# Kernel tuning notes

Hardware: AMD Instinct MI355X
Metric: run time of the kernel (lower is better)

## Reference

```python
import jax, jax.numpy as jnp
import numpy as np

N = 8192        # num nodes, > sparse_attention_threshold=5000 -> sparse attention path
IN = 128        # in_channels
OUT = 128       # out_channels
HEADS = 2       # attention_heads
DEG = 32        # avg degree used to build theta sparsity


def _xavier(key, shape):
    a = np.sqrt(6.0 / (shape[0] + shape[1])).astype(np.float32)
    return jax.random.uniform(key, shape, jnp.float32, -a, a)


def setup_inputs() -> dict:
    rng = np.random.default_rng(0)
    rows = np.repeat(np.arange(N), DEG)
    cols = rng.integers(0, N, size=N * DEG)
    theta_np = np.zeros((N, N), dtype=np.float32)
    theta_np[rows, cols] = 1.0
    # matches torch: rows, cols = np.where(theta > 1e-5)
    r, c = np.nonzero(theta_np > 1e-5)
    edge_index = jnp.asarray(np.stack([r, c]).astype(np.int32))  # [2, E]
    key = jax.random.key(0)
    ks = jax.random.split(key, 4)
    x = jax.random.normal(ks[0], (N, IN), jnp.float32)
    weight = _xavier(ks[1], (IN, OUT * HEADS))
    bias = jnp.zeros((OUT * HEADS,), jnp.float32)
    att_weight1 = _xavier(ks[2], (2 * OUT, OUT // 2))
    att_weight2 = _xavier(ks[3], (OUT // 2, 1))
    return {"x": x, "theta": jnp.asarray(theta_np), "weight": weight,
            "bias": bias, "att_weight1": att_weight1,
            "att_weight2": att_weight2, "edge_index": edge_index}


def _forward(x, weight, bias, att_weight1, att_weight2, edge_index):
    # x @ W + b, reshape to [N, heads, out]
    h = (x @ weight + bias).reshape(N, HEADS, OUT)
    src, dst = edge_index[0], edge_index[1]
    # cat([h_src, h_dst]) @ W1 == h_src @ W1[:OUT] + h_dst @ W1[OUT:]
    # project at node level first (cheaper), then gather per edge
    p_src = jnp.einsum('nhd,df->nhf', h, att_weight1[:OUT])
    p_dst = jnp.einsum('nhd,df->nhf', h, att_weight1[OUT:])
    s = jax.nn.leaky_relu(p_src[src] + p_dst[dst])               # [E, H, OUT//2]
    scores = jnp.einsum('ehf,fo->eho', s, att_weight2)[..., 0]    # [E, H]
    # torch does F.softmax(att_scores, dim=0): GLOBAL softmax over all edges per head
    att = jax.nn.softmax(scores, axis=0)                          # [E, H]
    # sparse COO mm: out[src] += att * h[dst]
    msgs = att[:, :, None] * h[dst]                               # [E, H, OUT]
    agg = jnp.zeros((N, HEADS, OUT), h.dtype).at[src].add(msgs)
    return agg.mean(axis=1)                                       # mean over heads -> [N, OUT]


def reference(x, theta, weight, bias, att_weight1, att_weight2, edge_index):
    # theta only determines the edge list (computed on CPU/numpy in the torch
    # code); edge_index is precomputed consistently in setup_inputs.
    del theta
    return _forward(x, weight, bias, att_weight1, att_weight2, edge_index)
```

## Files before the change

kernel.cpp:

```cpp
#include <hip/hip_runtime.h>
#include <hip/hip_bf16.h>

#define NN 8192
#define INC 128
#define HC 256
#define NPB 16
#define NGRP (NN / NPB)
#define APB 4
#define AGRID (NN / APB)
#define SCALE_BLOCKS 512
#define MAXDEG 32

__global__ __launch_bounds__(256) void k_h_p(
    const float* __restrict__ x, const float* __restrict__ W,
    const float* __restrict__ bias, const float* __restrict__ att1,
    const int* __restrict__ ei, float* __restrict__ h,
    float* __restrict__ ps, float* __restrict__ pd,
    int* __restrict__ offs, int E) {
  int t = threadIdx.x;
  int n0 = blockIdx.x * NPB;
  for (int e = blockIdx.x * 256 + t; e < E; e += NGRP * 256) {
    if (e == 0) offs[0] = 0;
    else { int s1 = ei[e]; if (s1 != ei[e - 1]) offs[s1] = e; }
    if (e == E - 1) offs[NN] = E;
  }
  __shared__ float xs[NPB * INC];
  __shared__ float hs[NPB * HC];
  {
    const float4* xin = (const float4*)(x + (size_t)n0 * INC);
    ((float4*)xs)[t] = xin[t];
    ((float4*)xs)[t + 256] = xin[t + 256];
  }
  __syncthreads();
  int cg = t & 63, ng = t >> 6;
  {
    float4 b4 = *(const float4*)&bias[cg * 4];
    float4 a0 = b4, a1 = b4, a2 = b4, a3 = b4;
    const float* xr0 = xs + (ng * 4 + 0) * INC;
    const float* xr1 = xs + (ng * 4 + 1) * INC;
    const float* xr2 = xs + (ng * 4 + 2) * INC;
    const float* xr3 = xs + (ng * 4 + 3) * INC;
    #pragma unroll 2
    for (int d = 0; d < INC; d += 4) {
      float4 xv0 = *(const float4*)&xr0[d];
      float4 xv1 = *(const float4*)&xr1[d];
      float4 xv2 = *(const float4*)&xr2[d];
      float4 xv3 = *(const float4*)&xr3[d];
      const float* f0 = (const float*)&xv0;
      const float* f1 = (const float*)&xv1;
      const float* f2 = (const float*)&xv2;
      const float* f3 = (const float*)&xv3;
      #pragma unroll
      for (int k = 0; k < 4; ++k) {
        float4 w4 = *(const float4*)&W[(size_t)(d + k) * HC + cg * 4];
        float x0 = f0[k], x1 = f1[k], x2 = f2[k], x3 = f3[k];
        a0.x += x0 * w4.x; a0.y += x0 * w4.y; a0.z += x0 * w4.z; a0.w += x0 * w4.w;
        a1.x += x1 * w4.x; a1.y += x1 * w4.y; a1.z += x1 * w4.z; a1.w += x1 * w4.w;
        a2.x += x2 * w4.x; a2.y += x2 * w4.y; a2.z += x2 * w4.z; a2.w += x2 * w4.w;
        a3.x += x3 * w4.x; a3.y += x3 * w4.y; a3.z += x3 * w4.z; a3.w += x3 * w4.w;
      }
    }
    float4* hb = (float4*)&hs[(ng * 4) * HC + cg * 4];
    *(float4*)&h[(size_t)(n0 + ng * 4 + 0) * HC + cg * 4] = a0;
    *(float4*)&h[(size_t)(n0 + ng * 4 + 1) * HC + cg * 4] = a1;
    *(float4*)&h[(size_t)(n0 + ng * 4 + 2) * HC + cg * 4] = a2;
    *(float4*)&h[(size_t)(n0 + ng * 4 + 3) * HC + cg * 4] = a3;
    hb[0] = a0; hb[HC / 4] = a1; hb[2 * HC / 4] = a2; hb[3 * HC / 4] = a3;
  }
  __syncthreads();
  {
    int fg = cg & 15, sel = cg >> 4;
    int head = sel & 1, isdst = sel >> 1;
    const float* a1p = att1 + isdst * 128 * 64 + fg * 4;
    float4 p0 = {0,0,0,0}, p1 = {0,0,0,0}, p2 = {0,0,0,0}, p3 = {0,0,0,0};
    const float* hr0 = hs + (ng * 4 + 0) * HC + head * 128;
    const float* hr1 = hs + (ng * 4 + 1) * HC + head * 128;
    const float* hr2 = hs + (ng * 4 + 2) * HC + head * 128;
    const float* hr3 = hs + (ng * 4 + 3) * HC + head * 128;
    #pragma unroll 2
    for (int d = 0; d < 128; d += 4) {
      float4 hv0 = *(const float4*)&hr0[d];
      float4 hv1 = *(const float4*)&hr1[d];
      float4 hv2 = *(const float4*)&hr2[d];
      float4 hv3 = *(const float4*)&hr3[d];
      const float* g0 = (const float*)&hv0;
      const float* g1 = (const float*)&hv1;
      const float* g2 = (const float*)&hv2;
      const float* g3 = (const float*)&hv3;
      #pragma unroll
      for (int k = 0; k < 4; ++k) {
        float4 a4 = *(const float4*)&a1p[(size_t)(d + k) * 64];
        float h0 = g0[k], h1 = g1[k], h2 = g2[k], h3 = g3[k];
        p0.x += h0 * a4.x; p0.y += h0 * a4.y; p0.z += h0 * a4.z; p0.w += h0 * a4.w;
        p1.x += h1 * a4.x; p1.y += h1 * a4.y; p1.z += h1 * a4.z; p1.w += h1 * a4.w;
        p2.x += h2 * a4.x; p2.y += h2 * a4.y; p2.z += h2 * a4.z; p2.w += h2 * a4.w;
        p3.x += h3 * a4.x; p3.y += h3 * a4.y; p3.z += h3 * a4.z; p3.w += h3 * a4.w;
      }
    }
    float* dp = isdst ? pd : ps;
    *(float4*)&dp[(size_t)(n0 + ng * 4 + 0) * 128 + head * 64 + fg * 4] = p0;
    *(float4*)&dp[(size_t)(n0 + ng * 4 + 1) * 128 + head * 64 + fg * 4] = p1;
    *(float4*)&dp[(size_t)(n0 + ng * 4 + 2) * 128 + head * 64 + fg * 4] = p2;
    *(float4*)&dp[(size_t)(n0 + ng * 4 + 3) * 128 + head * 64 + fg * 4] = p3;
  }
}

__global__ __launch_bounds__(256) void k_agg(
    const float* __restrict__ h, const float* __restrict__ ps,
    const float* __restrict__ pd, const int* __restrict__ ei,
    const float* __restrict__ att2, const int* __restrict__ offs,
    float* __restrict__ raw, float* __restrict__ part, int E) {
  int t = threadIdx.x, wid = t >> 6, lane = t & 63;
  int n = blockIdx.x * APB + wid;
  __shared__ float w2l[64];
  __shared__ int   dstl[APB][MAXDEG];
  if (t < 64) w2l[t] = att2[t];
  int lo = offs[n], hi = offs[n + 1];
  int m = hi - lo;
  if (lane < m) dstl[wid][lane] = ei[E + lo + lane];
  __syncthreads();
  int head = lane >> 5, j = lane & 31;
  float2 psv = *(const float2*)&ps[(size_t)n * 128 + head * 64 + j * 2];
  float wa = w2l[j * 2], wb = w2l[j * 2 + 1];
  float rsum = 0.f;
  float4 a0 = {0, 0, 0, 0}, a1 = {0, 0, 0, 0};
  int i = 0;
  #pragma unroll 2
  for (; i + 2 <= m; i += 2) {
    int d0 = dstl[wid][i], d1 = dstl[wid][i + 1];
    float2 q0 = *(const float2*)&pd[(size_t)d0 * 128 + head * 64 + j * 2];
    float2 q1 = *(const float2*)&pd[(size_t)d1 * 128 + head * 64 + j * 2];
    float4 h0 = *(const float4*)&h[(size_t)d0 * HC + lane * 4];
    float4 h1 = *(const float4*)&h[(size_t)d1 * HC + lane * 4];
    float u0 = psv.x + q0.x; u0 = u0 > 0.f ? u0 : 0.01f * u0;
    float u1 = psv.y + q0.y; u1 = u1 > 0.f ? u1 : 0.01f * u1;
    float s0 = u0 * wa + u1 * wb;
    float v0 = psv.x + q1.x; v0 = v0 > 0.f ? v0 : 0.01f * v0;
    float v1 = psv.y + q1.y; v1 = v1 > 0.f ? v1 : 0.01f * v1;
    float s1 = v0 * wa + v1 * wb;
    s0 += __shfl_xor(s0, 1);  s0 += __shfl_xor(s0, 2);  s0 += __shfl_xor(s0, 4);
    s0 += __shfl_xor(s0, 8);  s0 += __shfl_xor(s0, 16);
    s1 += __shfl_xor(s1, 1);  s1 += __shfl_xor(s1, 2);  s1 += __shfl_xor(s1, 4);
    s1 += __shfl_xor(s1, 8);  s1 += __shfl_xor(s1, 16);
    float e0 = __expf(s0), e1 = __expf(s1);
    rsum += e0; rsum += e1;
    a0.x += e0 * h0.x; a0.y += e0 * h0.y; a0.z += e0 * h0.z; a0.w += e0 * h0.w;
    a1.x += e1 * h1.x; a1.y += e1 * h1.y; a1.z += e1 * h1.z; a1.w += e1 * h1.w;
  }
  if (i < m) {
    int d0 = dstl[wid][i];
    float2 q0 = *(const float2*)&pd[(size_t)d0 * 128 + head * 64 + j * 2];
    float4 h0 = *(const float4*)&h[(size_t)d0 * HC + lane * 4];
    float u0 = psv.x + q0.x; u0 = u0 > 0.f ? u0 : 0.01f * u0;
    float u1 = psv.y + q0.y; u1 = u1 > 0.f ? u1 : 0.01f * u1;
    float s0 = u0 * wa + u1 * wb;
    s0 += __shfl_xor(s0, 1);  s0 += __shfl_xor(s0, 2);  s0 += __shfl_xor(s0, 4);
    s0 += __shfl_xor(s0, 8);  s0 += __shfl_xor(s0, 16);
    float e0 = __expf(s0);
    rsum += e0;
    a0.x += e0 * h0.x; a0.y += e0 * h0.y; a0.z += e0 * h0.z; a0.w += e0 * h0.w;
  }
  if (j == 0) part[n * 2 + head] = rsum;
  float4 res;
  res.x = a0.x + a1.x; res.y = a0.y + a1.y;
  res.z = a0.z + a1.z; res.w = a0.w + a1.w;
  *(float4*)&raw[(size_t)n * HC + lane * 4] = res;
}

__global__ __launch_bounds__(256) void k_scale(
    const float* __restrict__ raw, const float* __restrict__ part,
    float* __restrict__ out) {
  int t = threadIdx.x;
  float s0 = 0.f, s1 = 0.f;
  #pragma unroll 4
  for (int k = 0; k < 32; ++k) {
    float2 p = ((const float2*)part)[t + 256 * k];
    s0 += p.x; s1 += p.y;
  }
  #pragma unroll
  for (int off = 1; off <= 32; off <<= 1) {
    s0 += __shfl_xor(s0, off);
    s1 += __shfl_xor(s1, off);
  }
  __shared__ float ws0[4], ws1[4];
  if ((t & 63) == 0) { ws0[t >> 6] = s0; ws1[t >> 6] = s1; }
  __syncthreads();
  float inv0 = 1.f / (ws0[0] + ws0[1] + ws0[2] + ws0[3]);
  float inv1 = 1.f / (ws1[0] + ws1[1] + ws1[2] + ws1[3]);
  const float4* r4 = (const float4*)raw;
  float4* o4 = (float4*)out;
  int idx = blockIdx.x * 256 + t;
  #pragma unroll
  for (int rep = 0; rep < 2; ++rep, idx += SCALE_BLOCKS * 256) {
    int nn = idx >> 5, c4 = idx & 31;
    float4 a = r4[nn * 64 + c4];
    float4 b = r4[nn * 64 + 32 + c4];
    float4 o;
    o.x = 0.5f * (a.x * inv0 + b.x * inv1);
    o.y = 0.5f * (a.y * inv0 + b.y * inv1);
    o.z = 0.5f * (a.z * inv0 + b.z * inv1);
    o.w = 0.5f * (a.w * inv0 + b.w * inv1);
    o4[idx] = o;
  }
}

extern "C" void kernel_launch(void* const* d_in, const int* in_sizes, int n_in,
                              void* d_out, int out_size, void* d_ws, size_t ws_size,
                              hipStream_t stream) {
  const float* x    = (const float*)d_in[0];
  const float* W    = (const float*)d_in[2];
  const float* bias = (const float*)d_in[3];
  const float* att1 = (const float*)d_in[4];
  const float* att2 = (const float*)d_in[5];
  const int* ei = (const int*)d_in[6];
  int E = in_sizes[6] / 2;
  float* out = (float*)d_out;

  float* ws = (float*)d_ws;
  float* h    = ws;
  float* ps   = h  + (size_t)NN * HC;
  float* pd   = ps + (size_t)NN * 128;
  float* raw  = pd + (size_t)NN * 128;
  float* part = raw + (size_t)NN * HC;
  int*   offs = (int*)(part + (size_t)NN * 2);

  k_h_p<<<NGRP, 256, 0, stream>>>(x, W, bias, att1, ei, h, ps, pd, offs, E);
  k_agg<<<AGRID, 256, 0, stream>>>(h, ps, pd, ei, att2, offs, raw, part, E);
  k_scale<<<SCALE_BLOCKS, 256, 0, stream>>>(raw, part, out);
}
```

Measured before the change: 364.6 us.

## Split aggregation across head and channel-half blocks with XCD-aware mapping

The aggregation kernel now launches four times as many blocks, each handling one (head, channel-half) pair for a group of nodes, so each wave lane holds one scalar channel instead of a float4. Block indices are decoded so that all blocks on a given XCD (bid & 7) share the same head/channel combination, which is meant to keep that XCD's L2 working set to one column slice of h and pd. The cost is that the score computation, including the pd gather, is repeated for each channel half. Loads also shrink from float4 to scalar per lane.

```diff
diff --git a/kernel.cpp b/kernel.cpp
--- a/kernel.cpp
+++ b/kernel.cpp
@@ -7,7 +7,7 @@
 #define NPB 16
 #define NGRP (NN / NPB)
 #define APB 4
-#define AGRID (NN / APB)
+#define AGRID ((NN / APB) * 4)
 #define SCALE_BLOCKS 512
 #define MAXDEG 32
 
@@ -111,7 +111,12 @@
     const float* __restrict__ att2, const int* __restrict__ offs,
     float* __restrict__ raw, float* __restrict__ part, int E) {
   int t = threadIdx.x, wid = t >> 6, lane = t & 63;
-  int n = blockIdx.x * APB + wid;
+  int bid = blockIdx.x;
+  int xcd = bid & 7;
+  int combo = xcd >> 1;
+  int head = combo >> 1, ch = combo & 1;
+  int gidx = ((bid >> 3) << 1) | (xcd & 1);
+  int n = gidx * APB + wid;
   __shared__ float w2l[64];
   __shared__ int   dstl[APB][MAXDEG];
   if (t < 64) w2l[t] = att2[t];
@@ -119,52 +124,45 @@
   int m = hi - lo;
   if (lane < m) dstl[wid][lane] = ei[E + lo + lane];
   __syncthreads();
-  int head = lane >> 5, j = lane & 31;
-  float2 psv = *(const float2*)&ps[(size_t)n * 128 + head * 64 + j * 2];
-  float wa = w2l[j * 2], wb = w2l[j * 2 + 1];
+  float psv = ps[(size_t)n * 128 + head * 64 + lane];
+  float wa  = w2l[lane];
+  const float* pdc  = pd + head * 64 + lane;
+  const float* hcol = h + head * 128 + ch * 64 + lane;
   float rsum = 0.f;
-  float4 a0 = {0, 0, 0, 0}, a1 = {0, 0, 0, 0};
+  float a0 = 0.f, a1 = 0.f;
   int i = 0;
   #pragma unroll 2
   for (; i + 2 <= m; i += 2) {
     int d0 = dstl[wid][i], d1 = dstl[wid][i + 1];
-    float2 q0 = *(const float2*)&pd[(size_t)d0 * 128 + head * 64 + j * 2];
-    float2 q1 = *(const float2*)&pd[(size_t)d1 * 128 + head * 64 + j * 2];
-    float4 h0 = *(const float4*)&h[(size_t)d0 * HC + lane * 4];
-    float4 h1 = *(const float4*)&h[(size_t)d1 * HC + lane * 4];
-    float u0 = psv.x + q0.x; u0 = u0 > 0.f ? u0 : 0.01f * u0;
-    float u1 = psv.y + q0.y; u1 = u1 > 0.f ? u1 : 0.01f * u1;
-    float s0 = u0 * wa + u1 * wb;
-    float v0 = psv.x + q1.x; v0 = v0 > 0.f ? v0 : 0.01f * v0;
-    float v1 = psv.y + q1.y; v1 = v1 > 0.f ? v1 : 0.01f * v1;
-    float s1 = v0 * wa + v1 * wb;
+    float q0 = pdc[(size_t)d0 * 128];
+    float q1 = pdc[(size_t)d1 * 128];
+    float g0 = hcol[(size_t)d0 * HC];
+    float g1 = hcol[(size_t)d1 * HC];
+    float u0 = psv + q0; u0 = u0 > 0.f ? u0 : 0.01f * u0;
+    float u1 = psv + q1; u1 = u1 > 0.f ? u1 : 0.01f * u1;
+    float s0 = u0 * wa, s1 = u1 * wa;
     s0 += __shfl_xor(s0, 1);  s0 += __shfl_xor(s0, 2);  s0 += __shfl_xor(s0, 4);
-    s0 += __shfl_xor(s0, 8);  s0 += __shfl_xor(s0, 16);
+    s0 += __shfl_xor(s0, 8);  s0 += __shfl_xor(s0, 16); s0 += __shfl_xor(s0, 32);
     s1 += __shfl_xor(s1, 1);  s1 += __shfl_xor(s1, 2);  s1 += __shfl_xor(s1, 4);
-    s1 += __shfl_xor(s1, 8);  s1 += __shfl_xor(s1, 16);
+    s1 += __shfl_xor(s1, 8);  s1 += __shfl_xor(s1, 16); s1 += __shfl_xor(s1, 32);
     float e0 = __expf(s0), e1 = __expf(s1);
     rsum += e0; rsum += e1;
-    a0.x += e0 * h0.x; a0.y += e0 * h0.y; a0.z += e0 * h0.z; a0.w += e0 * h0.w;
-    a1.x += e1 * h1.x; a1.y += e1 * h1.y; a1.z += e1 * h1.z; a1.w += e1 * h1.w;
+    a0 += e0 * g0; a1 += e1 * g1;
   }
   if (i < m) {
     int d0 = dstl[wid][i];
-    float2 q0 = *(const float2*)&pd[(size_t)d0 * 128 + head * 64 + j * 2];
-    float4 h0 = *(const float4*)&h[(size_t)d0 * HC + lane * 4];
-    float u0 = psv.x + q0.x; u0 = u0 > 0.f ? u0 : 0.01f * u0;
-    float u1 = psv.y + q0.y; u1 = u1 > 0.f ? u1 : 0.01f * u1;
-    float s0 = u0 * wa + u1 * wb;
+    float q0 = pdc[(size_t)d0 * 128];
+    float g0 = hcol[(size_t)d0 * HC];
+    float u0 = psv + q0; u0 = u0 > 0.f ? u0 : 0.01f * u0;
+    float s0 = u0 * wa;
     s0 += __shfl_xor(s0, 1);  s0 += __shfl_xor(s0, 2);  s0 += __shfl_xor(s0, 4);
-    s0 += __shfl_xor(s0, 8);  s0 += __shfl_xor(s0, 16);
+    s0 += __shfl_xor(s0, 8);  s0 += __shfl_xor(s0, 16); s0 += __shfl_xor(s0, 32);
     float e0 = __expf(s0);
     rsum += e0;
-    a0.x += e0 * h0.x; a0.y += e0 * h0.y; a0.z += e0 * h0.z; a0.w += e0 * h0.w;
-  }
-  if (j == 0) part[n * 2 + head] = rsum;
-  float4 res;
-  res.x = a0.x + a1.x; res.y = a0.y + a1.y;
-  res.z = a0.z + a1.z; res.w = a0.w + a1.w;
-  *(float4*)&raw[(size_t)n * HC + lane * 4] = res;
+    a0 += e0 * g0;
+  }
+  if (ch == 0 && lane == 0) part[n * 2 + head] = rsum;
+  raw[(size_t)n * HC + head * 128 + ch * 64 + lane] = a0 + a1;
 }
 
 __global__ __launch_bounds__(256) void k_scale(
```

New measurement: 402.8 us. +10.5%, slower.
